# Kernel tuning notes

Hardware: AMD Instinct MI355X
Metric: run time of the kernel (lower is better)

## Reference

```python
import jax, jax.numpy as jnp
import numpy as np

B, T, S, D, V, NX = 4, 256, 400, 512, 50000, 50
VEXT = V + NX  # extended vocab


def setup_inputs() -> dict:
    key = jax.random.key(0)
    ks = jax.random.split(key, 10)
    s = 0.02
    return {
        "x": jax.random.normal(ks[0], (B, T, D), dtype=jnp.float32),
        "enc_outputs": jax.random.normal(ks[1], (B, S, D), dtype=jnp.float32),
        "src_mask": jax.random.randint(ks[2], (B, 1, S), 0, 2, dtype=jnp.int32),
        "enc_batch_extend_vocab": jax.random.randint(ks[3], (B, S), 0, VEXT, dtype=jnp.int64),
        "extra_zeros": jnp.zeros((B, T, NX), dtype=jnp.float32),
        "fc_w": jax.random.normal(ks[4], (V, D), dtype=jnp.float32) * s,
        "fc_b": jnp.zeros((V,), dtype=jnp.float32),
        "pgen_w": jax.random.normal(ks[5], (1, D), dtype=jnp.float32) * s,
        "pgen_b": jnp.zeros((1,), dtype=jnp.float32),
        "wq": jax.random.normal(ks[6], (D, D), dtype=jnp.float32) * s,
        "bq": jnp.zeros((D,), dtype=jnp.float32),
        "wk": jax.random.normal(ks[7], (D, D), dtype=jnp.float32) * s,
        "bk": jnp.zeros((D,), dtype=jnp.float32),
    }


def reference(x, enc_outputs, src_mask, enc_batch_extend_vocab, extra_zeros,
              fc_w, fc_b, pgen_w, pgen_b, wq, bq, wk, bk):
    # vocab distribution: [B,T,V]
    p_vocab = jax.nn.softmax(x @ fc_w.T + fc_b, axis=-1)
    # single-head cross attention probs (h=1 -> d_k = D)
    q = x @ wq.T + bq                 # [B,T,D]
    k = enc_outputs @ wk.T + bk       # [B,S,D]
    scores = jnp.einsum('btd,bsd->bts', q, k) / jnp.sqrt(jnp.float32(D))
    scores = jnp.where(src_mask == 0, jnp.float32(-1e9), scores)  # mask [B,1,S]
    attn_probs = jax.nn.softmax(scores, axis=-1)  # [B,T,S]
    # generation gate
    p_gen = jax.nn.sigmoid(x @ pgen_w.T + pgen_b)  # [B,T,1]
    attn_dist = (1.0 - p_gen) * attn_probs         # copy distribution over source
    p_ext = jnp.concatenate([p_gen * p_vocab, extra_zeros], axis=-1)  # [B,T,VEXT]
    # scatter-add copy probs into extended vocab slots
    b_idx = jnp.arange(B)[:, None, None]
    t_idx = jnp.arange(T)[None, :, None]
    v_idx = enc_batch_extend_vocab[:, None, :]
    bb, tt, vv = jnp.broadcast_arrays(b_idx, t_idx, v_idx)  # each [B,T,S]
    p_ext = p_ext.at[bb, tt, vv].add(attn_dist)
    return jnp.log(jnp.maximum(p_ext, jnp.float32(1e-9)))
```

## Files before the change

kernel.cpp:

```cpp
#include <hip/hip_runtime.h>
#include <hip/hip_bf16.h>
#include <math.h>

constexpr int cB = 4, cT = 256, cS = 400, cD = 512, cV = 50000, cNX = 50;
constexpr int cVEXT = cV + cNX;
constexpr int cPAN2 = (cV + 255) / 256;
constexpr int cCBLD = cVEXT * 2;
constexpr int cTOP  = 50100;
constexpr int cMQ   = cB * cT;

typedef __attribute__((ext_vector_type(8))) short short8v;
typedef __attribute__((ext_vector_type(4))) float floatx4;

__device__ inline ushort f2bf(float f) {
    union { float f; unsigned u; } v; v.f = f;
    unsigned r = (v.u + 0x7FFFu + ((v.u >> 16) & 1u)) >> 16;
    return (ushort)r;
}
__device__ inline float bf2f(ushort u) {
    union { unsigned u; float f; } v; v.u = ((unsigned)u) << 16;
    return v.f;
}

__global__ __launch_bounds__(256) void cast_kernel(
    const float* __restrict__ src, ushort* __restrict__ dst, int n4)
{
    const int stride = gridDim.x * 256;
    for (int i = blockIdx.x * 256 + threadIdx.x; i < n4; i += stride) {
        float4 v = *(const float4*)(src + (size_t)i * 4);
        ushort4 o;
        o.x = f2bf(v.x); o.y = f2bf(v.y); o.z = f2bf(v.z); o.w = f2bf(v.w);
        *(ushort4*)(dst + (size_t)i * 4) = o;
    }
}

__global__ __launch_bounds__(256) void gemm_proj(
    const ushort* __restrict__ A, const ushort* __restrict__ Wb,
    const float* __restrict__ bias, float* __restrict__ Cf,
    int M, int N, int K, int ldc)
{
    __shared__ ushort As[2][128 * 32];
    __shared__ ushort Bs[2][128 * 32];

    const int tid  = threadIdx.x;
    const int lane = tid & 63;
    const int wv   = tid >> 6;
    const int wm   = wv >> 1;
    const int wn   = wv & 1;
    const int bm   = blockIdx.x * 128;
    const int bn   = blockIdx.y * 128;

    const int rA = lane & 15;
    const int kA = (lane >> 4) * 8;
    const int nt = K >> 5;

    floatx4 acc[4][4] = {};

    auto stage = [&](int bidx, int t) {
        const int k0 = t * 32;
        #pragma unroll
        for (int c = 0; c < 2; ++c) {
            const int chunk = wv * 2 + c;
            int ga = bm + chunk * 16 + rA; if (ga >= M) ga = M - 1;
            __builtin_amdgcn_global_load_lds(
                (const __attribute__((address_space(1))) void*)(A + (size_t)ga * K + k0 + kA),
                (__attribute__((address_space(3))) void*)&As[bidx][chunk * 512], 16, 0, 0);
            int gb = bn + chunk * 16 + rA; if (gb >= N) gb = N - 1;
            __builtin_amdgcn_global_load_lds(
                (const __attribute__((address_space(1))) void*)(Wb + (size_t)gb * K + k0 + kA),
                (__attribute__((address_space(3))) void*)&Bs[bidx][chunk * 512], 16, 0, 0);
        }
    };

    stage(0, 0);
    __syncthreads();

    int buf = 0;
    for (int t = 0; t < nt; ++t) {
        if (t + 1 < nt) stage(buf ^ 1, t + 1);
        short8v a[4], b[4];
        #pragma unroll
        for (int mi = 0; mi < 4; ++mi)
            a[mi] = *(const short8v*)&As[buf][(wm * 4 + mi) * 512 + lane * 8];
        #pragma unroll
        for (int ni = 0; ni < 4; ++ni)
            b[ni] = *(const short8v*)&Bs[buf][(wn * 4 + ni) * 512 + lane * 8];
        #pragma unroll
        for (int mi = 0; mi < 4; ++mi)
            #pragma unroll
            for (int ni = 0; ni < 4; ++ni)
                acc[mi][ni] = __builtin_amdgcn_mfma_f32_16x16x32_bf16(
                    a[mi], b[ni], acc[mi][ni], 0, 0, 0);
        __syncthreads();
        buf ^= 1;
    }

    const int fr = lane & 15;
    const int g  = lane >> 4;
    #pragma unroll
    for (int mi = 0; mi < 4; ++mi) {
        #pragma unroll
        for (int ni = 0; ni < 4; ++ni) {
            const int colg = bn + wn * 64 + ni * 16 + fr;
            if (colg >= N) continue;
            const float bv = bias[colg];
            #pragma unroll
            for (int r = 0; r < 4; ++r) {
                const int row = bm + wm * 64 + mi * 16 + g * 4 + r;
                if (row < M) Cf[(size_t)row * ldc + colg] = acc[mi][ni][r] + bv;
            }
        }
    }
}

__global__ __launch_bounds__(512) void gemm_big(
    const ushort* __restrict__ A, const ushort* __restrict__ Wb,
    const float* __restrict__ bias, ushort* __restrict__ Cb,
    float* __restrict__ pm, float* __restrict__ ps)
{
    __shared__ ushort As[2][8 * 512];
    __shared__ ushort Bs[2][16 * 512];
    __shared__ float sm_m[4][128];
    __shared__ float sm_s[4][128];

    const int tid  = threadIdx.x;
    const int lane = tid & 63;
    const int wv   = tid >> 6;
    const int wm   = wv >> 2;
    const int wn   = wv & 3;

    const int wg  = blockIdx.y * gridDim.x + blockIdx.x;
    const int nwg = gridDim.x * gridDim.y;
    const int j   = (wg & 7) * (nwg >> 3) + (wg >> 3);
    const int pan = j >> 3;
    const int bm  = (j & 7) * 128;
    const int bn  = pan * 256;

    const int rA = lane & 15;
    const int kA = (lane >> 4) * 8;

    floatx4 acc[4][4] = {};

    auto stage = [&](int bidx, int t) {
        const int k0 = t * 32;
        {
            const int ga = bm + wv * 16 + rA;
            __builtin_amdgcn_global_load_lds(
                (const __attribute__((address_space(1))) void*)(A + (size_t)ga * cD + k0 + kA),
                (__attribute__((address_space(3))) void*)&As[bidx][wv * 512], 16, 0, 0);
        }
        #pragma unroll
        for (int c = 0; c < 2; ++c) {
            const int chunk = wv * 2 + c;
            int gb = bn + chunk * 16 + rA; if (gb >= cV) gb = cV - 1;
            __builtin_amdgcn_global_load_lds(
                (const __attribute__((address_space(1))) void*)(Wb + (size_t)gb * cD + k0 + kA),
                (__attribute__((address_space(3))) void*)&Bs[bidx][chunk * 512], 16, 0, 0);
        }
    };

    stage(0, 0);
    __syncthreads();

    int buf = 0;
    #pragma unroll 1
    for (int t = 0; t < 16; ++t) {
        if (t + 1 < 16) stage(buf ^ 1, t + 1);
        short8v a[4], b[4];
        #pragma unroll
        for (int mi = 0; mi < 4; ++mi)
            a[mi] = *(const short8v*)&As[buf][(wm * 4 + mi) * 512 + lane * 8];
        #pragma unroll
        for (int ni = 0; ni < 4; ++ni)
            b[ni] = *(const short8v*)&Bs[buf][(wn * 4 + ni) * 512 + lane * 8];
        #pragma unroll
        for (int mi = 0; mi < 4; ++mi)
            #pragma unroll
            for (int ni = 0; ni < 4; ++ni)
                acc[mi][ni] = __builtin_amdgcn_mfma_f32_16x16x32_bf16(
                    a[mi], b[ni], acc[mi][ni], 0, 0, 0);
        __syncthreads();
        buf ^= 1;
    }

    const int fr = lane & 15;
    const int g  = lane >> 4;

    float bv[4]; bool val[4];
    #pragma unroll
    for (int ni = 0; ni < 4; ++ni) {
        const int colg = bn + wn * 64 + ni * 16 + fr;
        val[ni] = (colg < cV);
        bv[ni] = val[ni] ? bias[colg] : 0.f;
    }
    #pragma unroll
    for (int mi = 0; mi < 4; ++mi)
        #pragma unroll
        for (int ni = 0; ni < 4; ++ni)
            #pragma unroll
            for (int r = 0; r < 4; ++r)
                acc[mi][ni][r] += bv[ni];

    #pragma unroll
    for (int mi = 0; mi < 4; ++mi) {
        #pragma unroll
        for (int r = 0; r < 4; ++r) {
            float mx = -1e30f;
            #pragma unroll
            for (int ni = 0; ni < 4; ++ni)
                if (val[ni]) mx = fmaxf(mx, acc[mi][ni][r]);
            #pragma unroll
            for (int sw = 1; sw < 16; sw <<= 1)
                mx = fmaxf(mx, __shfl_xor(mx, sw));
            float sm = 0.f;
            #pragma unroll
            for (int ni = 0; ni < 4; ++ni)
                if (val[ni]) sm += __expf(acc[mi][ni][r] - mx);
            #pragma unroll
            for (int sw = 1; sw < 16; sw <<= 1)
                sm += __shfl_xor(sm, sw);
            if (fr == 0) {
                const int rl = wm * 64 + mi * 16 + g * 4 + r;
                sm_m[wn][rl] = mx;
                sm_s[wn][rl] = sm;
            }
        }
    }
    __syncthreads();
    if (tid < 128) {
        float m = sm_m[0][tid], s = sm_s[0][tid];
        #pragma unroll
        for (int i = 1; i < 4; ++i) {
            const float m2 = sm_m[i][tid], s2 = sm_s[i][tid];
            const float nm = fmaxf(m, m2);
            s = s * __expf(m - nm) + s2 * __expf(m2 - nm);
            m = nm;
        }
        const int grow = bm + tid;
        pm[(size_t)pan * cMQ + grow] = m;
        ps[(size_t)pan * cMQ + grow] = s;
    }

    #pragma unroll
    for (int mi = 0; mi < 4; ++mi) {
        #pragma unroll
        for (int ni = 0; ni < 4; ++ni) {
            if (!val[ni]) continue;
            const int colg = bn + wn * 64 + ni * 16 + fr;
            #pragma unroll
            for (int r = 0; r < 4; ++r) {
                const int row = bm + wm * 64 + mi * 16 + g * 4 + r;
                Cb[(size_t)row * cCBLD + cTOP + colg] = f2bf(acc[mi][ni][r]);
            }
        }
    }
}

__global__ __launch_bounds__(256) void combine_kernel(
    const float* __restrict__ pm, const float* __restrict__ ps,
    const float* __restrict__ pgen, float* __restrict__ rowadd)
{
    const int lane = threadIdx.x & 63;
    const int wv   = threadIdx.x >> 6;
    const int row  = blockIdx.x * 64 + lane;

    float m = -1e30f, s = 0.f;
    #pragma unroll 2
    for (int i = wv; i < cPAN2; i += 4) {
        const float mi = pm[(size_t)i * cMQ + row];
        const float si = ps[(size_t)i * cMQ + row];
        const float nm = fmaxf(m, mi);
        s = s * __expf(m - nm) + si * __expf(mi - nm);
        m = nm;
    }
    __shared__ float rm[4][64], rs[4][64];
    rm[wv][lane] = m; rs[wv][lane] = s;
    __syncthreads();
    if (wv == 0) {
        m = rm[0][lane]; s = rs[0][lane];
        #pragma unroll
        for (int i = 1; i < 4; ++i) {
            const float m2 = rm[i][lane], s2 = rs[i][lane];
            const float nm = fmaxf(m, m2);
            s = s * __expf(m - nm) + s2 * __expf(m2 - nm);
            m = nm;
        }
        rowadd[row] = __logf(pgen[row]) - m - __logf(s);
    }
}

__global__ __launch_bounds__(512) void transform_reg(
    float* __restrict__ out, const float* __restrict__ rowadd,
    const int* __restrict__ ebev, const float* __restrict__ attn)
{
    const int row = blockIdx.x;
    const int b   = row / cT;
    const int tid = threadIdx.x;
    constexpr float LOGMIN = -20.72326583694641f;
    constexpr int NCHUNK = cV / 8;

    __shared__ int   pos[cS];
    __shared__ float add[cS];
    for (int s = tid; s < cS; s += 512) {
        pos[s] = ebev[b * cS + s];
        add[s] = attn[(size_t)row * cS + s];
    }

    const float a = rowadd[row];
    const ushort* rowu = (const ushort*)out + (size_t)row * cCBLD + cTOP;
    float* rowf = out + (size_t)row * cVEXT;

    ushort4 lo[13], hi[13];
    #pragma unroll
    for (int t = 0; t < 13; ++t) {
        const int cidx = t * 512 + tid;
        if (cidx < NCHUNK) {
            lo[t] = *(const ushort4*)(rowu + (size_t)cidx * 8);
            hi[t] = *(const ushort4*)(rowu + (size_t)cidx * 8 + 4);
        }
    }
    __syncthreads();

    #pragma unroll
    for (int t = 0; t < 13; ++t) {
        const int cidx = t * 512 + tid;
        if (cidx < NCHUNK) {
            const int jb = cidx * 8;
            float2 o;
            o.x = fmaxf(bf2f(lo[t].x) + a, LOGMIN);
            o.y = fmaxf(bf2f(lo[t].y) + a, LOGMIN);
            *(float2*)(rowf + jb) = o;
            o.x = fmaxf(bf2f(lo[t].z) + a, LOGMIN);
            o.y = fmaxf(bf2f(lo[t].w) + a, LOGMIN);
            *(float2*)(rowf + jb + 2) = o;
            o.x = fmaxf(bf2f(hi[t].x) + a, LOGMIN);
            o.y = fmaxf(bf2f(hi[t].y) + a, LOGMIN);
            *(float2*)(rowf + jb + 4) = o;
            o.x = fmaxf(bf2f(hi[t].z) + a, LOGMIN);
            o.y = fmaxf(bf2f(hi[t].w) + a, LOGMIN);
            *(float2*)(rowf + jb + 6) = o;
        }
    }
    if (tid < (cVEXT - cV) / 2) {
        float2 z; z.x = LOGMIN; z.y = LOGMIN;
        *(float2*)(rowf + cV + 2 * tid) = z;
    }
    __syncthreads();

    for (int s = tid; s < cS; s += 512) {
        const int p = pos[s];
        bool leader = true;
        for (int s2 = 0; s2 < s; ++s2)
            if (pos[s2] == p) { leader = false; break; }
        if (!leader) continue;
        float sum = add[s];
        for (int s2 = s + 1; s2 < cS; ++s2)
            if (pos[s2] == p) sum += add[s2];
        const float base = __expf(rowf[p]);
        rowf[p] = __logf(fmaxf(base + sum, 1e-9f));
    }
}

__global__ __launch_bounds__(64) void pgen_kernel(
    const float* __restrict__ x, const float* __restrict__ w,
    const float* __restrict__ b, float* __restrict__ pgen)
{
    const int row = blockIdx.x;
    const int lane = threadIdx.x;
    const float* xr = x + (size_t)row * cD;
    float s = 0.f;
    for (int i = lane; i < cD; i += 64) s += xr[i] * w[i];
    #pragma unroll
    for (int off = 32; off; off >>= 1) s += __shfl_down(s, off);
    if (lane == 0) pgen[row] = 1.f / (1.f + __expf(-(s + b[0])));
}

__global__ __launch_bounds__(256) void attn_kernel(
    const float* __restrict__ q, const float* __restrict__ k,
    const int* __restrict__ src_mask, const float* __restrict__ pgen,
    float* __restrict__ attn)
{
    constexpr float scale = 0.04419417382415922f;
    const int row = blockIdx.x;
    const int b = row / cT;
    const int tid = threadIdx.x;

    __shared__ __align__(16) float qs[cD];
    __shared__ float sc[cS];
    __shared__ float red[4];

    for (int i = tid; i < cD; i += 256) qs[i] = q[(size_t)row * cD + i];
    __syncthreads();

    for (int s = tid; s < cS; s += 256) {
        const float* kr = k + ((size_t)b * cS + s) * cD;
        float dot = 0.f;
        #pragma unroll 4
        for (int i = 0; i < cD; i += 4) {
            float4 kv = *(const float4*)(kr + i);
            float4 qv = *(const float4*)(qs + i);
            dot += qv.x * kv.x + qv.y * kv.y + qv.z * kv.z + qv.w * kv.w;
        }
        float v = dot * scale;
        if (src_mask[b * cS + s] == 0) v = -1e9f;
        sc[s] = v;
    }
    __syncthreads();

    float m = -3.4e38f;
    for (int s = tid; s < cS; s += 256) m = fmaxf(m, sc[s]);
    #pragma unroll
    for (int off = 32; off; off >>= 1) m = fmaxf(m, __shfl_down(m, off));
    if ((tid & 63) == 0) red[tid >> 6] = m;
    __syncthreads();
    m = fmaxf(fmaxf(red[0], red[1]), fmaxf(red[2], red[3]));
    __syncthreads();

    float sum = 0.f;
    for (int s = tid; s < cS; s += 256) {
        float e = __expf(sc[s] - m);
        sc[s] = e;
        sum += e;
    }
    #pragma unroll
    for (int off = 32; off; off >>= 1) sum += __shfl_down(sum, off);
    if ((tid & 63) == 0) red[tid >> 6] = sum;
    __syncthreads();
    sum = red[0] + red[1] + red[2] + red[3];

    const float w = (1.f - pgen[row]) / sum;
    for (int s = tid; s < cS; s += 256)
        attn[(size_t)row * cS + s] = sc[s] * w;
}

extern "C" void kernel_launch(void* const* d_in, const int* in_sizes, int n_in,
                              void* d_out, int out_size, void* d_ws, size_t ws_size,
                              hipStream_t stream)
{
    const float* x      = (const float*)d_in[0];
    const float* enc    = (const float*)d_in[1];
    const int*   mask   = (const int*)d_in[2];
    const int*   ebev   = (const int*)d_in[3];
    const float* fc_w   = (const float*)d_in[5];
    const float* fc_b   = (const float*)d_in[6];
    const float* pgen_w = (const float*)d_in[7];
    const float* pgen_b = (const float*)d_in[8];
    const float* wq     = (const float*)d_in[9];
    const float* bq     = (const float*)d_in[10];
    const float* wk     = (const float*)d_in[11];
    const float* bk     = (const float*)d_in[12];
    float* out = (float*)d_out;

    float* ws     = (float*)d_ws;
    float* q      = ws;
    float* kbuf   = q + (size_t)cB * cT * cD;
    float* pgen   = kbuf + (size_t)cB * cS * cD;
    float* attn   = pgen + cB * cT;
    float* pm     = attn + (size_t)cB * cT * cS;
    float* ps     = pm + (size_t)cPAN2 * cMQ;
    float* rowadd = ps + (size_t)cPAN2 * cMQ;
    ushort* xb    = (ushort*)(rowadd + cMQ);
    ushort* encb  = xb + (size_t)cB * cT * cD;
    ushort* wqb   = encb + (size_t)cB * cS * cD;
    ushort* wkb   = wqb + (size_t)cD * cD;
    ushort* wb    = wkb + (size_t)cD * cD;

    const dim3 blk(256);
    const int MQ = cMQ;
    const int MK = cB * cS;

    cast_kernel<<<dim3(512), blk, 0, stream>>>(x, xb, (cB * cT * cD) / 4);
    cast_kernel<<<dim3(512), blk, 0, stream>>>(enc, encb, (cB * cS * cD) / 4);
    cast_kernel<<<dim3(256), blk, 0, stream>>>(wq, wqb, (cD * cD) / 4);
    cast_kernel<<<dim3(256), blk, 0, stream>>>(wk, wkb, (cD * cD) / 4);
    cast_kernel<<<dim3(2048), blk, 0, stream>>>(fc_w, wb, (cV * cD) / 4);

    gemm_proj<<<dim3(MQ / 128, cD / 128), blk, 0, stream>>>(
        xb, wqb, bq, q, MQ, cD, cD, cD);
    gemm_proj<<<dim3((MK + 127) / 128, cD / 128), blk, 0, stream>>>(
        encb, wkb, bk, kbuf, MK, cD, cD, cD);
    pgen_kernel<<<dim3(MQ), dim3(64), 0, stream>>>(x, pgen_w, pgen_b, pgen);

    attn_kernel<<<dim3(MQ), blk, 0, stream>>>(q, kbuf, mask, pgen, attn);

    gemm_big<<<dim3(8, cPAN2), dim3(512), 0, stream>>>(
        xb, wb, fc_b, (ushort*)out, pm, ps);

    combine_kernel<<<dim3(MQ / 64), blk, 0, stream>>>(pm, ps, pgen, rowadd);

    transform_reg<<<dim3(MQ), dim3(512), 0, stream>>>(out, rowadd, ebev, attn);
}
```

Baseline: 423.3 us.

## Shrink big GEMM tile to 128x128 with 256 threads and batch transform loads

The vocab GEMM moves from 128x256 tiles with 8 waves to 128x128 tiles with 4 waves. The LDS staging layout changes to row-major 32-wide K rows, and the grid doubles along N. The per-tile softmax partials now merge 2 column waves instead of 4, and the combine kernel reduces over twice as many panels. Separately, the transform kernel loads and writes in four batches instead of holding all 13 chunks in registers, which should reduce register pressure at the cost of extra barriers.

```diff
diff --git a/kernel.cpp b/kernel.cpp
--- a/kernel.cpp
+++ b/kernel.cpp
@@ -4,7 +4,7 @@
 
 constexpr int cB = 4, cT = 256, cS = 400, cD = 512, cV = 50000, cNX = 50;
 constexpr int cVEXT = cV + cNX;
-constexpr int cPAN2 = (cV + 255) / 256;
+constexpr int cPAN  = (cV + 127) / 128;
 constexpr int cCBLD = cVEXT * 2;
 constexpr int cTOP  = 50100;
 constexpr int cMQ   = cB * cT;
@@ -113,66 +113,71 @@
     }
 }
 
-__global__ __launch_bounds__(512) void gemm_big(
+__global__ __launch_bounds__(256) void gemm_big(
     const ushort* __restrict__ A, const ushort* __restrict__ Wb,
     const float* __restrict__ bias, ushort* __restrict__ Cb,
     float* __restrict__ pm, float* __restrict__ ps)
 {
-    __shared__ ushort As[2][8 * 512];
-    __shared__ ushort Bs[2][16 * 512];
-    __shared__ float sm_m[4][128];
-    __shared__ float sm_s[4][128];
+    __shared__ ushort As[2][128 * 32];
+    __shared__ ushort Bs[2][128 * 32];
+    __shared__ float sm_m[2][128];
+    __shared__ float sm_s[2][128];
 
     const int tid  = threadIdx.x;
     const int lane = tid & 63;
     const int wv   = tid >> 6;
-    const int wm   = wv >> 2;
-    const int wn   = wv & 3;
+    const int wm   = wv >> 1;
+    const int wn   = wv & 1;
 
     const int wg  = blockIdx.y * gridDim.x + blockIdx.x;
     const int nwg = gridDim.x * gridDim.y;
     const int j   = (wg & 7) * (nwg >> 3) + (wg >> 3);
     const int pan = j >> 3;
     const int bm  = (j & 7) * 128;
-    const int bn  = pan * 256;
-
-    const int rA = lane & 15;
-    const int kA = (lane >> 4) * 8;
+    const int bn  = pan * 128;
+
+    const int srow = lane >> 2;
+    const int sk   = (lane & 3) * 8;
 
     floatx4 acc[4][4] = {};
 
     auto stage = [&](int bidx, int t) {
         const int k0 = t * 32;
-        {
-            const int ga = bm + wv * 16 + rA;
+        #pragma unroll
+        for (int c = 0; c < 2; ++c) {
+            const int lr = wv * 32 + c * 16;
+            const int ga = bm + lr + srow;
             __builtin_amdgcn_global_load_lds(
-                (const __attribute__((address_space(1))) void*)(A + (size_t)ga * cD + k0 + kA),
-                (__attribute__((address_space(3))) void*)&As[bidx][wv * 512], 16, 0, 0);
+                (const __attribute__((address_space(1))) void*)(A + (size_t)ga * cD + k0 + sk),
+                (__attribute__((address_space(3))) void*)&As[bidx][lr * 32], 16, 0, 0);
         }
         #pragma unroll
         for (int c = 0; c < 2; ++c) {
-            const int chunk = wv * 2 + c;
-            int gb = bn + chunk * 16 + rA; if (gb >= cV) gb = cV - 1;
+            const int lr = wv * 32 + c * 16;
+            int gb = bn + lr + srow; if (gb >= cV) gb = cV - 1;
             __builtin_amdgcn_global_load_lds(
-                (const __attribute__((address_space(1))) void*)(Wb + (size_t)gb * cD + k0 + kA),
-                (__attribute__((address_space(3))) void*)&Bs[bidx][chunk * 512], 16, 0, 0);
+                (const __attribute__((address_space(1))) void*)(Wb + (size_t)gb * cD + k0 + sk),
+                (__attribute__((address_space(3))) void*)&Bs[bidx][lr * 32], 16, 0, 0);
         }
     };
 
     stage(0, 0);
     __syncthreads();
 
+    const int fr = lane & 15;
+    const int g  = lane >> 4;
     int buf = 0;
+
     #pragma unroll 1
     for (int t = 0; t < 16; ++t) {
         if (t + 1 < 16) stage(buf ^ 1, t + 1);
         short8v a[4], b[4];
         #pragma unroll
         for (int mi = 0; mi < 4; ++mi)
-            a[mi] = *(const short8v*)&As[buf][(wm * 4 + mi) * 512 + lane * 8];
+            a[mi] = *(const short8v*)&As[buf][(wm * 64 + mi * 16 + fr) * 32 + g * 8];
         #pragma unroll
         for (int ni = 0; ni < 4; ++ni)
-            b[ni] = *(const short8v*)&Bs[buf][(wn * 4 + ni) * 512 + lane * 8];
+            b[ni] = *(const short8v*)&Bs[buf][(wn * 64 + ni * 16 + fr) * 32 + g * 8];
         #pragma unroll
         for (int mi = 0; mi < 4; ++mi)
             #pragma unroll
@@ -182,9 +187,6 @@
         __syncthreads();
         buf ^= 1;
     }
-
-    const int fr = lane & 15;
-    const int g  = lane >> 4;
 
     float bv[4]; bool val[4];
     #pragma unroll
@@ -228,17 +230,13 @@
     }
     __syncthreads();
     if (tid < 128) {
-        float m = sm_m[0][tid], s = sm_s[0][tid];
-        #pragma unroll
-        for (int i = 1; i < 4; ++i) {
-            const float m2 = sm_m[i][tid], s2 = sm_s[i][tid];
-            const float nm = fmaxf(m, m2);
-            s = s * __expf(m - nm) + s2 * __expf(m2 - nm);
-            m = nm;
-        }
+        const float m0 = sm_m[0][tid], m1 = sm_m[1][tid];
+        const float s0 = sm_s[0][tid], s1 = sm_s[1][tid];
+        const float mm = fmaxf(m0, m1);
+        const float ss = s0 * __expf(m0 - mm) + s1 * __expf(m1 - mm);
         const int grow = bm + tid;
-        pm[(size_t)pan * cMQ + grow] = m;
-        ps[(size_t)pan * cMQ + grow] = s;
+        pm[(size_t)pan * cMQ + grow] = mm;
+        ps[(size_t)pan * cMQ + grow] = ss;
     }
 
     #pragma unroll
@@ -266,7 +264,7 @@
 
     float m = -1e30f, s = 0.f;
     #pragma unroll 2
-    for (int i = wv; i < cPAN2; i += 4) {
+    for (int i = wv; i < cPAN; i += 4) {
         const float mi = pm[(size_t)i * cMQ + row];
         const float si = ps[(size_t)i * cMQ + row];
         const float nm = fmaxf(m, mi);
@@ -310,35 +308,44 @@
     const ushort* rowu = (const ushort*)out + (size_t)row * cCBLD + cTOP;
     float* rowf = out + (size_t)row * cVEXT;
 
-    ushort4 lo[13], hi[13];
-    #pragma unroll
-    for (int t = 0; t < 13; ++t) {
-        const int cidx = t * 512 + tid;
-        if (cidx < NCHUNK) {
-            lo[t] = *(const ushort4*)(rowu + (size_t)cidx * 8);
-            hi[t] = *(const ushort4*)(rowu + (size_t)cidx * 8 + 4);
-        }
-    }
-    __syncthreads();
-
-    #pragma unroll
-    for (int t = 0; t < 13; ++t) {
-        const int cidx = t * 512 + tid;
-        if (cidx < NCHUNK) {
-            const int jb = cidx * 8;
-            float2 o;
-            o.x = fmaxf(bf2f(lo[t].x) + a, LOGMIN);
-            o.y = fmaxf(bf2f(lo[t].y) + a, LOGMIN);
-            *(float2*)(rowf + jb) = o;
-            o.x = fmaxf(bf2f(lo[t].z) + a, LOGMIN);
-            o.y = fmaxf(bf2f(lo[t].w) + a, LOGMIN);
-            *(float2*)(rowf + jb + 2) = o;
-            o.x = fmaxf(bf2f(hi[t].x) + a, LOGMIN);
-            o.y = fmaxf(bf2f(hi[t].y) + a, LOGMIN);
-            *(float2*)(rowf + jb + 4) = o;
-            o.x = fmaxf(bf2f(hi[t].z) + a, LOGMIN);
-            o.y = fmaxf(bf2f(hi[t].w) + a, LOGMIN);
-            *(float2*)(rowf + jb + 6) = o;
+    constexpr int BLO[5] = {0, 4, 7, 10, 13};
+    #pragma unroll
+    for (int bb = 0; bb < 4; ++bb) {
+        ushort4 lo[4], hi[4];
+        #pragma unroll
+        for (int s = 0; s < 4; ++s) {
+            const int t = BLO[bb] + s;
+            if (t < BLO[bb + 1]) {
+                const int cidx = t * 512 + tid;
+                if (cidx < NCHUNK) {
+                    lo[s] = *(const ushort4*)(rowu + (size_t)cidx * 8);
+                    hi[s] = *(const ushort4*)(rowu + (size_t)cidx * 8 + 4);
+                }
+            }
+        }
+        __syncthreads();
+        #pragma unroll
+        for (int s = 0; s < 4; ++s) {
+            const int t = BLO[bb] + s;
+            if (t < BLO[bb + 1]) {
+                const int cidx = t * 512 + tid;
+                if (cidx < NCHUNK) {
+                    const int jb = cidx * 8;
+                    float2 o;
+                    o.x = fmaxf(bf2f(lo[s].x) + a, LOGMIN);
+                    o.y = fmaxf(bf2f(lo[s].y) + a, LOGMIN);
+                    *(float2*)(rowf + jb) = o;
+                    o.x = fmaxf(bf2f(lo[s].z) + a, LOGMIN);
+                    o.y = fmaxf(bf2f(lo[s].w) + a, LOGMIN);
+                    *(float2*)(rowf + jb + 2) = o;
+                    o.x = fmaxf(bf2f(hi[s].x) + a, LOGMIN);
+                    o.y = fmaxf(bf2f(hi[s].y) + a, LOGMIN);
+                    *(float2*)(rowf + jb + 4) = o;
+                    o.x = fmaxf(bf2f(hi[s].z) + a, LOGMIN);
+                    o.y = fmaxf(bf2f(hi[s].w) + a, LOGMIN);
+                    *(float2*)(rowf + jb + 6) = o;
+                }
+            }
         }
     }
     if (tid < (cVEXT - cV) / 2) {
@@ -457,8 +464,8 @@
     float* pgen   = kbuf + (size_t)cB * cS * cD;
     float* attn   = pgen + cB * cT;
     float* pm     = attn + (size_t)cB * cT * cS;
-    float* ps     = pm + (size_t)cPAN2 * cMQ;
-    float* rowadd = ps + (size_t)cPAN2 * cMQ;
+    float* ps     = pm + (size_t)cPAN * cMQ;
+    float* rowadd = ps + (size_t)cPAN * cMQ;
     ushort* xb    = (ushort*)(rowadd + cMQ);
     ushort* encb  = xb + (size_t)cB * cT * cD;
     ushort* wqb   = encb + (size_t)cB * cS * cD;
@@ -483,7 +490,7 @@
 
     attn_kernel<<<dim3(MQ), blk, 0, stream>>>(q, kbuf, mask, pgen, attn);
 
-    gemm_big<<<dim3(8, cPAN2), dim3(512), 0, stream>>>(
+    gemm_big<<<dim3(8, cPAN), blk, 0, stream>>>(
         xb, wb, fc_b, (ushort*)out, pm, ps);
 
     combine_kernel<<<dim3(MQ / 64), blk, 0, stream>>>(pm, ps, pgen, rowadd);
```

Measured after the change: 414.8 us. 1.02x faster.
